# Performance work log

Hardware: AMD Instinct MI355X
Metric: run time of the kernel (lower is better)

The kernel has to match this reference:

```python
import jax, jax.numpy as jnp
import numpy as np

EPS = 1e-5


def _whiten(X, T):
    # X: (B, C, H, W); group whitening with g=1, d=C, m=B*H*W
    B, C, H, W = X.shape
    g, d = 1, C
    x = jnp.transpose(X, (1, 0, 2, 3)).reshape(g, d, -1)  # (g, d, m)
    m = x.shape[-1]
    mean = jnp.mean(x, axis=-1, keepdims=True)
    xc = x - mean
    I = jnp.broadcast_to(jnp.eye(d, dtype=X.dtype)[None], (g, d, d))
    Sigma = EPS * I + jnp.einsum('gim,gjm->gij', xc, xc) / m
    rTr = 1.0 / jnp.trace(Sigma, axis1=1, axis2=2)[:, None, None]  # 1/tr(Sigma)
    Sigma_N = Sigma * rTr
    P = I
    for _ in range(T):  # Newton-Schulz: P <- 1.5*P - 0.5*P^3 @ Sigma_N
        P = 1.5 * P - 0.5 * (P @ P @ P @ Sigma_N)
    wm = P * jnp.sqrt(rTr)  # inverse sqrt of Sigma
    xn = jnp.einsum('gij,gjm->gim', wm, xc)  # (g, d, m)
    return jnp.transpose(xn.reshape(C, B, H, W), (1, 0, 2, 3))


def reference(X, rot, T):
    # mode = -1: whiten then rotate with running_rot, affine=False
    B, C, H, W = X.shape
    g = rot.shape[0]
    d = C // g
    Xn = _whiten(X, T)                       # (B, C, H, W)
    Xh = Xn.reshape(B, g, d, H, W)
    Xr = jnp.einsum('bgchw,gdc->bgdhw', Xh, rot)
    return Xr.reshape(B, C, H, W)


def setup_inputs() -> dict:
    key = jax.random.key(0)
    k1, k2 = jax.random.split(key)
    X = jax.random.normal(k1, (32, 512, 56, 56), dtype=jnp.float32)
    # running_rot buffer; use a random orthogonal matrix for realism
    A = jax.random.normal(k2, (512, 512), dtype=jnp.float32)
    Q, _ = jnp.linalg.qr(A)
    rot = Q[None]  # (1, 512, 512)
    return {"X": X, "rot": rot, "T": 10}
```

## Files before the change

### kernel.cpp

```cpp
#include <hip/hip_runtime.h>
#include <hip/hip_bf16.h>

typedef __bf16 v8bf __attribute__((ext_vector_type(8)));
typedef float  v4f  __attribute__((ext_vector_type(4)));
typedef unsigned short u16;
typedef unsigned int   u32;

#define GAS __attribute__((address_space(1)))
#define LAS __attribute__((address_space(3)))

constexpr int C_ = 512;
constexpr int S_ = 3136;
constexpr int B_ = 32;
constexpr int M_ = B_ * S_;
constexpr float INV_M = 1.0f / (float)M_;

__device__ __forceinline__ void async16(const u16* g, u16* l) {
  __builtin_amdgcn_global_load_lds((const GAS u32*)g, (LAS u32*)l, 16, 0, 0);
}

__device__ __forceinline__ u16 f2bf(float f) {
  u32 u = __builtin_bit_cast(u32, f);
  u += 0x7fffu + ((u >> 16) & 1u);
  return (u16)(u >> 16);
}
__device__ __forceinline__ float bf2f(u16 h) {
  u32 u = ((u32)h) << 16;
  return __builtin_bit_cast(float, u);
}

__global__ __launch_bounds__(256) void prep_kernel(const float* __restrict__ X,
        u16* __restrict__ xbf, u16* __restrict__ xbfT, float* __restrict__ chsum) {
  __shared__ u16 Ts[64 * 65];
  const int tid = threadIdx.x;
  const int s0 = blockIdx.x * 64;
  const int c0 = blockIdx.y * 64;
  const int b  = blockIdx.z;

  const int i  = tid >> 2;
  const int jc = (tid & 3) * 16;
  const float* xp = X + (b * C_ + c0 + i) * S_ + s0 + jc;
  u16* op = xbf + (c0 + i) * M_ + b * S_ + s0 + jc;
  float ssum = 0.f;
  #pragma unroll
  for (int u = 0; u < 4; ++u) {
    float4 xv = *(const float4*)(xp + u * 4);
    ssum += xv.x + xv.y + xv.z + xv.w;
    u16 e0 = f2bf(xv.x), e1 = f2bf(xv.y), e2 = f2bf(xv.z), e3 = f2bf(xv.w);
    *(ushort4*)(op + u * 4) = make_ushort4(e0, e1, e2, e3);
    const int lb = i * 65 + jc + u * 4;
    Ts[lb + 0] = e0; Ts[lb + 1] = e1; Ts[lb + 2] = e2; Ts[lb + 3] = e3;
  }
  ssum += __shfl_down(ssum, 2, 4);
  ssum += __shfl_down(ssum, 1, 4);
  if ((tid & 3) == 0) atomicAdd(&chsum[c0 + i], ssum);
  __syncthreads();

  const int lane = tid & 63, wv = tid >> 6;
  #pragma unroll
  for (int p = 0; p < 2; ++p) {
    const int j  = p * 32 + wv * 8 + (lane >> 3);
    const int cc = (lane & 7) * 8;
    u16 tmp[8];
    #pragma unroll
    for (int e = 0; e < 8; ++e) tmp[e] = Ts[(cc + e) * 65 + j];
    u16* tp = xbfT + (b * S_ + s0 + j) * C_ + c0 + cc;
    *(ushort4*)(tp + 0) = make_ushort4(tmp[0], tmp[1], tmp[2], tmp[3]);
    *(ushort4*)(tp + 4) = make_ushort4(tmp[4], tmp[5], tmp[6], tmp[7]);
  }
}

__global__ __launch_bounds__(256, 2) void sigma_gemm(const u16* __restrict__ xbf,
                                                     float* __restrict__ part) {
  __shared__ u16 As[128 * 64];
  __shared__ u16 Bs[128 * 64];
  const int tid = threadIdx.x;
  const int bid = blockIdx.x;
  const int z = bid & 31;
  const int t = bid >> 5;
  const int ti = (t >= 9) ? 3 : (t >= 7) ? 2 : (t >= 4) ? 1 : 0;
  const int tb = (t >= 9) ? 9 : (t >= 7) ? 7 : (t >= 4) ? 4 : 0;
  const int tj = ti + (t - tb);
  const int kbase = z * S_;
  const int srow = tid >> 3;
  const int scol = (tid & 7) * 8;
  const int lane = tid & 63, wv = tid >> 6;
  const int wm = (wv & 1) * 64, wn = (wv >> 1) * 64;
  const int lr = lane & 15, lq = lane >> 4;
  const u16* gA = xbf + (ti * 128) * M_ + kbase + scol;
  const u16* gB = xbf + (tj * 128) * M_ + kbase + scol;
  v4f acc[4][4] = {};
  for (int it = 0; it < 49; ++it) {
    const int k0 = it * 64;
    #pragma unroll
    for (int q = 0; q < 4; ++q) {
      const int r = q * 32 + srow;
      async16(gA + r * M_ + k0, &As[r * 64 + scol]);
      async16(gB + r * M_ + k0, &Bs[r * 64 + scol]);
    }
    __syncthreads();
    #pragma unroll
    for (int kk = 0; kk < 2; ++kk) {
      v8bf a[4], b[4];
      #pragma unroll
      for (int x = 0; x < 4; ++x) a[x] = *(const v8bf*)&As[(wm + x*16 + lr)*64 + kk*32 + lq*8];
      #pragma unroll
      for (int x = 0; x < 4; ++x) b[x] = *(const v8bf*)&Bs[(wn + x*16 + lr)*64 + kk*32 + lq*8];
      #pragma unroll
      for (int mi = 0; mi < 4; ++mi)
        #pragma unroll
        for (int ni = 0; ni < 4; ++ni)
          acc[mi][ni] = __builtin_amdgcn_mfma_f32_16x16x32_bf16(a[mi], b[ni], acc[mi][ni], 0, 0, 0);
    }
    __syncthreads();
  }
  float* op = part + (size_t)(z * 10 + t) * (128 * 128);
  #pragma unroll
  for (int mi = 0; mi < 4; ++mi) {
    const int li = wm + mi * 16 + lq * 4;
    #pragma unroll
    for (int ni = 0; ni < 4; ++ni) {
      const int lj = wn + ni * 16 + lr;
      #pragma unroll
      for (int r = 0; r < 4; ++r)
        op[(li + r) * 128 + lj] = acc[mi][ni][r];
    }
  }
}

__global__ __launch_bounds__(256) void reduce_sigma(const float* __restrict__ part,
        const float* __restrict__ chsum, float* __restrict__ Sigma,
        float* __restrict__ trace) {
  const int idx = blockIdx.x * 256 + threadIdx.x;
  const int t = idx >> 14;
  const int r = idx & 16383;
  const int ii = r >> 7, jj = r & 127;
  const int ti = (t >= 9) ? 3 : (t >= 7) ? 2 : (t >= 4) ? 1 : 0;
  const int tb = (t >= 9) ? 9 : (t >= 7) ? 7 : (t >= 4) ? 4 : 0;
  const int tj = ti + (t - tb);
  const int i = ti * 128 + ii, j = tj * 128 + jj;
  float s = 0.f;
  #pragma unroll 8
  for (int z = 0; z < 32; ++z) s += part[(size_t)(z * 10 + t) * 16384 + r];
  float val = s * INV_M - (chsum[i] * INV_M) * (chsum[j] * INV_M);
  if (i == j) val += 1e-5f;
  Sigma[i * 512 + j] = val;
  if (i != j) Sigma[j * 512 + i] = val;
  if (i == j) atomicAdd(trace, val);
}

__global__ __launch_bounds__(256) void init_ns(const float* __restrict__ Sigma,
        const float* __restrict__ trace, const float* __restrict__ rot,
        u16* __restrict__ SNhi, u16* __restrict__ SNlo,
        float* __restrict__ P, u16* __restrict__ Phi, u16* __restrict__ Plo,
        u16* __restrict__ rothi, u16* __restrict__ rotlo) {
  const int idx = blockIdx.x * 256 + threadIdx.x;
  const float rtr = 1.0f / trace[0];
  const float sn = Sigma[idx] * rtr;
  u16 h = f2bf(sn);
  SNhi[idx] = h; SNlo[idx] = f2bf(sn - bf2f(h));
  const bool diag = (idx >> 9) == (idx & 511);
  P[idx] = diag ? 1.0f : 0.f;
  Phi[idx] = diag ? (u16)0x3F80 : (u16)0;
  Plo[idx] = 0;
  const float rv = rot[idx];
  u16 rh = f2bf(rv);
  rothi[idx] = rh; rotlo[idx] = f2bf(rv - bf2f(rh));
}

__global__ __launch_bounds__(256) void ns_mm(
    const u16* __restrict__ Ahi, const u16* __restrict__ Alo,
    const u16* __restrict__ B0hi, const u16* __restrict__ B0lo,
    const u16* __restrict__ B1hi, const u16* __restrict__ B1lo,
    u16* __restrict__ C0hi, u16* __restrict__ C0lo,
    u16* __restrict__ C1hi, u16* __restrict__ C1lo,
    float* __restrict__ P, const float* __restrict__ trace,
    float* __restrict__ M2f, u16* __restrict__ M2bf,
    const int* __restrict__ Tptr, int iter, int mode) {
  if (Tptr && iter >= Tptr[0]) return;
  __shared__ u16 Ah[64 * 64];
  __shared__ u16 Al[64 * 64];
  __shared__ u16 Bh[64 * 64];
  __shared__ u16 Bl[64 * 64];
  const int tid = threadIdx.x;
  const int tj = blockIdx.x, ti = blockIdx.y, zb = blockIdx.z;
  const u16* Bhip = zb ? B1hi : B0hi;
  const u16* Blop = zb ? B1lo : B0lo;
  const int r  = tid >> 3;
  const int sg = tid & 7;
  const int swz = (sg ^ (r & 7)) * 8;
  const int lofs = r * 64 + sg * 8;
  const u16* gAh = Ahi  + (ti * 64 + r) * 512 + swz;
  const u16* gAl = Alo  + (ti * 64 + r) * 512 + swz;
  const u16* gBh = Bhip + (tj * 64 + r) * 512 + swz;
  const u16* gBl = Blop + (tj * 64 + r) * 512 + swz;
  const int lane = tid & 63, wv = tid >> 6;
  const int wr = wv >> 1, wc = wv & 1;
  const int lr = lane & 15, lq = lane >> 4;
  v4f acc[2][2] = {};
  for (int it = 0; it < 8; ++it) {
    const int k0 = it * 64;
    async16(gAh + k0,            &Ah[lofs]);
    async16(gAh + k0 + 32 * 512, &Ah[lofs + 32 * 64]);
    async16(gAl + k0,            &Al[lofs]);
    async16(gAl + k0 + 32 * 512, &Al[lofs + 32 * 64]);
    async16(gBh + k0,            &Bh[lofs]);
    async16(gBh + k0 + 32 * 512, &Bh[lofs + 32 * 64]);
    async16(gBl + k0,            &Bl[lofs]);
    async16(gBl + k0 + 32 * 512, &Bl[lofs + 32 * 64]);
    __syncthreads();
    #pragma unroll
    for (int kk = 0; kk < 2; ++kk) {
      v8bf ah[2], al[2], bh[2], bl[2];
      const int col = ((kk * 4 + lq) ^ (lr & 7)) * 8;
      #pragma unroll
      for (int x = 0; x < 2; ++x) {
        const int rowA = (wr * 32 + x * 16 + lr) * 64;
        ah[x] = *(const v8bf*)&Ah[rowA + col];
        al[x] = *(const v8bf*)&Al[rowA + col];
        const int rowB = (wc * 32 + x * 16 + lr) * 64;
        bh[x] = *(const v8bf*)&Bh[rowB + col];
        bl[x] = *(const v8bf*)&Bl[rowB + col];
      }
      #pragma unroll
      for (int mi = 0; mi < 2; ++mi)
        #pragma unroll
        for (int ni = 0; ni < 2; ++ni) {
          acc[mi][ni] = __builtin_amdgcn_mfma_f32_16x16x32_bf16(ah[mi], bh[ni], acc[mi][ni], 0, 0, 0);
          acc[mi][ni] = __builtin_amdgcn_mfma_f32_16x16x32_bf16(ah[mi], bl[ni], acc[mi][ni], 0, 0, 0);
          acc[mi][ni] = __builtin_amdgcn_mfma_f32_16x16x32_bf16(al[mi], bh[ni], acc[mi][ni], 0, 0, 0);
        }
    }
    __syncthreads();
  }
  u16* Chi = zb ? C1hi : C0hi;
  u16* Clo = zb ? C1lo : C0lo;
  const float sc = (mode == 2) ? sqrtf(1.0f / trace[0]) : 0.f;
  #pragma unroll
  for (int mi = 0; mi < 2; ++mi) {
    const int gr0 = ti * 64 + wr * 32 + mi * 16 + lq * 4;
    #pragma unroll
    for (int ni = 0; ni < 2; ++ni) {
      const int gc = tj * 64 + wc * 32 + ni * 16 + lr;
      #pragma unroll
      for (int q = 0; q < 4; ++q) {
        const int o = (gr0 + q) * 512 + gc;
        const float vv = acc[mi][ni][q];
        if (mode == 0) {
          u16 h = f2bf(vv);
          Chi[o] = h; Clo[o] = f2bf(vv - bf2f(h));
        } else if (mode == 1) {
          const float nv = 1.5f * P[o] - 0.5f * vv;
          P[o] = nv;
          u16 h = f2bf(nv);
          Chi[o] = h; Clo[o] = f2bf(nv - bf2f(h));
        } else {
          const float w = vv * sc;
          M2f[o] = w; M2bf[o] = f2bf(w);
        }
      }
    }
  }
}

__global__ __launch_bounds__(256) void calc_v(const float* __restrict__ M2f,
        const float* __restrict__ chsum, float* __restrict__ v) {
  const int d = blockIdx.x * 256 + threadIdx.x;
  float s = 0.f;
  for (int c = 0; c < 512; ++c) s += M2f[d * 512 + c] * (chsum[c] * INV_M);
  v[d] = s;
}

__global__ __launch_bounds__(256, 2) void out_gemm(const u16* __restrict__ Abf,
        const u16* __restrict__ Bt, const float* __restrict__ v, float* __restrict__ out) {
  __shared__ u16 As[128 * 64];
  __shared__ u16 Bs[128 * 64];
  const int tid = threadIdx.x;
  const int tn = blockIdx.x, td = blockIdx.y;
  const int srow = tid >> 3, scol = (tid & 7) * 8;
  const int lane = tid & 63, wv = tid >> 6;
  const int wm = (wv & 1) * 64, wn = (wv >> 1) * 64;
  const int lr = lane & 15, lq = lane >> 4;
  const u16* gA = Abf + (td * 128) * 512 + scol;
  const u16* gB = Bt + (tn * 128) * 512 + scol;
  v4f acc[4][4] = {};
  for (int it = 0; it < 8; ++it) {
    const int k0 = it * 64;
    #pragma unroll
    for (int q = 0; q < 4; ++q) {
      const int r = q * 32 + srow;
      async16(gA + r * 512 + k0, &As[r * 64 + scol]);
      async16(gB + r * 512 + k0, &Bs[r * 64 + scol]);
    }
    __syncthreads();
    #pragma unroll
    for (int kk = 0; kk < 2; ++kk) {
      v8bf a[4], b[4];
      #pragma unroll
      for (int x = 0; x < 4; ++x) a[x] = *(const v8bf*)&As[(wm + x*16 + lr)*64 + kk*32 + lq*8];
      #pragma unroll
      for (int x = 0; x < 4; ++x) b[x] = *(const v8bf*)&Bs[(wn + x*16 + lr)*64 + kk*32 + lq*8];
      #pragma unroll
      for (int mi = 0; mi < 4; ++mi)
        #pragma unroll
        for (int ni = 0; ni < 4; ++ni)
          acc[mi][ni] = __builtin_amdgcn_mfma_f32_16x16x32_bf16(a[mi], b[ni], acc[mi][ni], 0, 0, 0);
    }
    __syncthreads();
  }
  #pragma unroll
  for (int mi = 0; mi < 4; ++mi) {
    const int d0 = td * 128 + wm + mi * 16 + lq * 4;
    const float vd0 = v[d0 + 0], vd1 = v[d0 + 1], vd2 = v[d0 + 2], vd3 = v[d0 + 3];
    #pragma unroll
    for (int ni = 0; ni < 4; ++ni) {
      const unsigned mcol = tn * 128 + wn + ni * 16 + lr;
      const unsigned bb = mcol / 3136u;
      const unsigned ss = mcol - bb * 3136u;
      const int obase = (int)(bb * 512u) * 3136 + (int)ss;
      out[obase + (d0 + 0) * 3136] = acc[mi][ni][0] - vd0;
      out[obase + (d0 + 1) * 3136] = acc[mi][ni][1] - vd1;
      out[obase + (d0 + 2) * 3136] = acc[mi][ni][2] - vd2;
      out[obase + (d0 + 3) * 3136] = acc[mi][ni][3] - vd3;
    }
  }
}

extern "C" void kernel_launch(void* const* d_in, const int* in_sizes, int n_in,
                              void* d_out, int out_size, void* d_ws, size_t ws_size,
                              hipStream_t stream) {
  const float* X   = (const float*)d_in[0];
  const float* rot = (const float*)d_in[1];
  const int*   T   = (const int*)d_in[2];
  float* out = (float*)d_out;

  char* ws = (char*)d_ws;
  size_t off = 0;
  auto alloc = [&](size_t bytes) -> char* {
    char* p = ws + off;
    off += (bytes + 255) & ~(size_t)255;
    return p;
  };
  u16*   xbf   = (u16*)alloc((size_t)C_ * M_ * 2);
  u16*   xbfT  = (u16*)alloc((size_t)M_ * C_ * 2);
  float* part  = (float*)alloc((size_t)320 * 16384 * 4);
  float* Sigma = (float*)alloc((size_t)C_ * C_ * 4);
  float* P     = (float*)alloc((size_t)C_ * C_ * 4);
  float* M2f   = (float*)alloc((size_t)C_ * C_ * 4);
  u16*   SNhi  = (u16*)alloc((size_t)C_ * C_ * 2);
  u16*   SNlo  = (u16*)alloc((size_t)C_ * C_ * 2);
  u16*   Phi   = (u16*)alloc((size_t)C_ * C_ * 2);
  u16*   Plo   = (u16*)alloc((size_t)C_ * C_ * 2);
  u16*   T1hi  = (u16*)alloc((size_t)C_ * C_ * 2);
  u16*   T1lo  = (u16*)alloc((size_t)C_ * C_ * 2);
  u16*   T2hi  = (u16*)alloc((size_t)C_ * C_ * 2);
  u16*   T2lo  = (u16*)alloc((size_t)C_ * C_ * 2);
  u16*   rothi = (u16*)alloc((size_t)C_ * C_ * 2);
  u16*   rotlo = (u16*)alloc((size_t)C_ * C_ * 2);
  u16*   M2bf  = (u16*)alloc((size_t)C_ * C_ * 2);
  float* chsum = (float*)alloc(2048);
  float* trace = (float*)alloc(256);
  float* v     = (float*)alloc(2048);
  (void)ws_size; (void)in_sizes; (void)n_in; (void)out_size;

  hipMemsetAsync(chsum, 0, 2048 + 256, stream);

  prep_kernel<<<dim3(49, 8, 32), 256, 0, stream>>>(X, xbf, xbfT, chsum);
  sigma_gemm<<<dim3(320), 256, 0, stream>>>(xbf, part);
  reduce_sigma<<<dim3(640), 256, 0, stream>>>(part, chsum, Sigma, trace);
  init_ns<<<dim3(1024), 256, 0, stream>>>(Sigma, trace, rot, SNhi, SNlo, P, Phi, Plo, rothi, rotlo);

  for (int iter = 0; iter < 10; ++iter) {
    ns_mm<<<dim3(8, 8, 2), 256, 0, stream>>>(Phi, Plo, Phi, Plo, SNhi, SNlo,
        T1hi, T1lo, T2hi, T2lo, P, trace, M2f, M2bf, T, iter, 0);
    ns_mm<<<dim3(8, 8, 1), 256, 0, stream>>>(T1hi, T1lo, T2hi, T2lo, nullptr, nullptr,
        Phi, Plo, nullptr, nullptr, P, trace, M2f, M2bf, T, iter, 1);
  }
  ns_mm<<<dim3(8, 8, 1), 256, 0, stream>>>(rothi, rotlo, Phi, Plo, nullptr, nullptr,
      Phi, Plo, nullptr, nullptr, P, trace, M2f, M2bf, nullptr, 0, 2);
  calc_v<<<dim3(2), 256, 0, stream>>>(M2f, chsum, v);
  out_gemm<<<dim3(784, 4), 256, 0, stream>>>(M2bf, xbfT, v, out);
}
```

Before: 805.0 us.

## Fuse Newton-Schulz iterations into one cooperative kernel with grid syncs

Replaces the reduce_sigma, init_ns, the twenty ns_mm launches and calc_v with a single cooperative kernel of 128 blocks that uses grid.sync between phases. The first Newton-Schulz iteration is folded analytically into initialization (P1 = 1.5I - 0.5*Sigma_N), which skips two matmuls. calc_v becomes a wave-parallel reduction with shuffles. The aim is to remove per-launch overhead and tail gaps in the small 512x512 iteration chain, at the cost of grid-wide barriers and half the blocks idling during single-output matmul phases.

```diff
diff --git a/kernel.cpp b/kernel.cpp
--- a/kernel.cpp
+++ b/kernel.cpp
@@ -1,5 +1,8 @@
 #include <hip/hip_runtime.h>
 #include <hip/hip_bf16.h>
+#include <hip/hip_cooperative_groups.h>
+
+namespace cg = cooperative_groups;
 
 typedef __bf16 v8bf __attribute__((ext_vector_type(8)));
 typedef float  v4f  __attribute__((ext_vector_type(4)));
@@ -128,78 +131,32 @@
   }
 }
 
-__global__ __launch_bounds__(256) void reduce_sigma(const float* __restrict__ part,
-        const float* __restrict__ chsum, float* __restrict__ Sigma,
-        float* __restrict__ trace) {
-  const int idx = blockIdx.x * 256 + threadIdx.x;
-  const int t = idx >> 14;
-  const int r = idx & 16383;
-  const int ii = r >> 7, jj = r & 127;
-  const int ti = (t >= 9) ? 3 : (t >= 7) ? 2 : (t >= 4) ? 1 : 0;
-  const int tb = (t >= 9) ? 9 : (t >= 7) ? 7 : (t >= 4) ? 4 : 0;
-  const int tj = ti + (t - tb);
-  const int i = ti * 128 + ii, j = tj * 128 + jj;
-  float s = 0.f;
-  #pragma unroll 8
-  for (int z = 0; z < 32; ++z) s += part[(size_t)(z * 10 + t) * 16384 + r];
-  float val = s * INV_M - (chsum[i] * INV_M) * (chsum[j] * INV_M);
-  if (i == j) val += 1e-5f;
-  Sigma[i * 512 + j] = val;
-  if (i != j) Sigma[j * 512 + i] = val;
-  if (i == j) atomicAdd(trace, val);
-}
-
-__global__ __launch_bounds__(256) void init_ns(const float* __restrict__ Sigma,
-        const float* __restrict__ trace, const float* __restrict__ rot,
-        u16* __restrict__ SNhi, u16* __restrict__ SNlo,
-        float* __restrict__ P, u16* __restrict__ Phi, u16* __restrict__ Plo,
-        u16* __restrict__ rothi, u16* __restrict__ rotlo) {
-  const int idx = blockIdx.x * 256 + threadIdx.x;
-  const float rtr = 1.0f / trace[0];
-  const float sn = Sigma[idx] * rtr;
-  u16 h = f2bf(sn);
-  SNhi[idx] = h; SNlo[idx] = f2bf(sn - bf2f(h));
-  const bool diag = (idx >> 9) == (idx & 511);
-  P[idx] = diag ? 1.0f : 0.f;
-  Phi[idx] = diag ? (u16)0x3F80 : (u16)0;
-  Plo[idx] = 0;
-  const float rv = rot[idx];
-  u16 rh = f2bf(rv);
-  rothi[idx] = rh; rotlo[idx] = f2bf(rv - bf2f(rh));
-}
-
-__global__ __launch_bounds__(256) void ns_mm(
+__device__ void mm64(
     const u16* __restrict__ Ahi, const u16* __restrict__ Alo,
-    const u16* __restrict__ B0hi, const u16* __restrict__ B0lo,
-    const u16* __restrict__ B1hi, const u16* __restrict__ B1lo,
-    u16* __restrict__ C0hi, u16* __restrict__ C0lo,
-    u16* __restrict__ C1hi, u16* __restrict__ C1lo,
-    float* __restrict__ P, const float* __restrict__ trace,
-    float* __restrict__ M2f, u16* __restrict__ M2bf,
-    const int* __restrict__ Tptr, int iter, int mode) {
-  if (Tptr && iter >= Tptr[0]) return;
+    const u16* __restrict__ Bhi, const u16* __restrict__ Blo,
+    int ti, int tj, int mode,
+    u16* __restrict__ Chi, u16* __restrict__ Clo,
+    float* __restrict__ P, float sc,
+    float* __restrict__ M2f, u16* __restrict__ M2bf) {
   __shared__ u16 Ah[64 * 64];
   __shared__ u16 Al[64 * 64];
   __shared__ u16 Bh[64 * 64];
   __shared__ u16 Bl[64 * 64];
   const int tid = threadIdx.x;
-  const int tj = blockIdx.x, ti = blockIdx.y, zb = blockIdx.z;
-  const u16* Bhip = zb ? B1hi : B0hi;
-  const u16* Blop = zb ? B1lo : B0lo;
   const int r  = tid >> 3;
   const int sg = tid & 7;
   const int swz = (sg ^ (r & 7)) * 8;
   const int lofs = r * 64 + sg * 8;
-  const u16* gAh = Ahi  + (ti * 64 + r) * 512 + swz;
-  const u16* gAl = Alo  + (ti * 64 + r) * 512 + swz;
-  const u16* gBh = Bhip + (tj * 64 + r) * 512 + swz;
-  const u16* gBl = Blop + (tj * 64 + r) * 512 + swz;
+  const u16* gAh = Ahi + (ti * 64 + r) * 512 + swz;
+  const u16* gAl = Alo + (ti * 64 + r) * 512 + swz;
+  const u16* gBh = Bhi + (tj * 64 + r) * 512 + swz;
+  const u16* gBl = Blo + (tj * 64 + r) * 512 + swz;
   const int lane = tid & 63, wv = tid >> 6;
   const int wr = wv >> 1, wc = wv & 1;
   const int lr = lane & 15, lq = lane >> 4;
   v4f acc[2][2] = {};
-  for (int it = 0; it < 8; ++it) {
-    const int k0 = it * 64;
+  for (int itk = 0; itk < 8; ++itk) {
+    const int k0 = itk * 64;
     async16(gAh + k0,            &Ah[lofs]);
     async16(gAh + k0 + 32 * 512, &Ah[lofs + 32 * 64]);
     async16(gAl + k0,            &Al[lofs]);
@@ -233,9 +190,6 @@
     }
     __syncthreads();
   }
-  u16* Chi = zb ? C1hi : C0hi;
-  u16* Clo = zb ? C1lo : C0lo;
-  const float sc = (mode == 2) ? sqrtf(1.0f / trace[0]) : 0.f;
   #pragma unroll
   for (int mi = 0; mi < 2; ++mi) {
     const int gr0 = ti * 64 + wr * 32 + mi * 16 + lq * 4;
@@ -263,12 +217,92 @@
   }
 }
 
-__global__ __launch_bounds__(256) void calc_v(const float* __restrict__ M2f,
-        const float* __restrict__ chsum, float* __restrict__ v) {
-  const int d = blockIdx.x * 256 + threadIdx.x;
-  float s = 0.f;
-  for (int c = 0; c < 512; ++c) s += M2f[d * 512 + c] * (chsum[c] * INV_M);
-  v[d] = s;
+__global__ __launch_bounds__(256) void ns_coop(
+    const float* __restrict__ part, const float* __restrict__ chsum,
+    float* __restrict__ Sigma, float* __restrict__ trace,
+    const float* __restrict__ rot,
+    u16* __restrict__ SNhi, u16* __restrict__ SNlo,
+    u16* __restrict__ Phi,  u16* __restrict__ Plo,
+    u16* __restrict__ T1hi, u16* __restrict__ T1lo,
+    u16* __restrict__ T2hi, u16* __restrict__ T2lo,
+    u16* __restrict__ rothi, u16* __restrict__ rotlo,
+    float* __restrict__ P, float* __restrict__ M2f, u16* __restrict__ M2bf,
+    float* __restrict__ v, const int* __restrict__ Tptr) {
+  cg::grid_group grid = cg::this_grid();
+  const int bid = blockIdx.x;
+  const int tid = threadIdx.x;
+  const int gidx0 = bid * 256 + tid;
+
+  for (int idx = gidx0; idx < 10 * 16384; idx += 128 * 256) {
+    const int t = idx >> 14;
+    const int rr = idx & 16383;
+    const int ii = rr >> 7, jj = rr & 127;
+    const int ti = (t >= 9) ? 3 : (t >= 7) ? 2 : (t >= 4) ? 1 : 0;
+    const int tb = (t >= 9) ? 9 : (t >= 7) ? 7 : (t >= 4) ? 4 : 0;
+    const int tj = ti + (t - tb);
+    const int i = ti * 128 + ii, j = tj * 128 + jj;
+    float s = 0.f;
+    #pragma unroll 8
+    for (int z = 0; z < 32; ++z) s += part[(size_t)(z * 10 + t) * 16384 + rr];
+    float val = s * INV_M - (chsum[i] * INV_M) * (chsum[j] * INV_M);
+    if (i == j) val += 1e-5f;
+    Sigma[i * 512 + j] = val;
+    if (i != j) Sigma[j * 512 + i] = val;
+    if (i == j) atomicAdd(trace, val);
+  }
+  grid.sync();
+
+  const float rtr = 1.0f / trace[0];
+  const int Tval = Tptr[0];
+
+  for (int idx = gidx0; idx < 512 * 512; idx += 128 * 256) {
+    const float sn = Sigma[idx] * rtr;
+    u16 h = f2bf(sn);
+    SNhi[idx] = h; SNlo[idx] = f2bf(sn - bf2f(h));
+    const bool diag = (idx >> 9) == (idx & 511);
+    const float p0 = (Tval > 0) ? ((diag ? 1.5f : 0.f) - 0.5f * sn)
+                                : (diag ? 1.0f : 0.f);
+    P[idx] = p0;
+    u16 ph = f2bf(p0);
+    Phi[idx] = ph; Plo[idx] = f2bf(p0 - bf2f(ph));
+    const float rv = rot[idx];
+    u16 rh = f2bf(rv);
+    rothi[idx] = rh; rotlo[idx] = f2bf(rv - bf2f(rh));
+  }
+  grid.sync();
+
+  for (int it = 1; it < Tval; ++it) {
+    {
+      const int job = bid & 63, zb = bid >> 6;
+      mm64(Phi, Plo, zb ? SNhi : Phi, zb ? SNlo : Plo,
+           job >> 3, job & 7, 0,
+           zb ? T2hi : T1hi, zb ? T2lo : T1lo, P, 0.f, M2f, M2bf);
+    }
+    grid.sync();
+    if (bid < 64) {
+      mm64(T1hi, T1lo, T2hi, T2lo, bid >> 3, bid & 7, 1,
+           Phi, Plo, P, 0.f, M2f, M2bf);
+    }
+    grid.sync();
+  }
+
+  if (bid < 64) {
+    mm64(rothi, rotlo, Phi, Plo, bid >> 3, bid & 7, 2,
+         nullptr, nullptr, P, sqrtf(rtr), M2f, M2bf);
+  }
+  grid.sync();
+
+  {
+    const int d = bid * 4 + (tid >> 6);
+    const int lane = tid & 63;
+    float s = 0.f;
+    for (int c = lane; c < 512; c += 64)
+      s += M2f[d * 512 + c] * (chsum[c] * INV_M);
+    s += __shfl_down(s, 32); s += __shfl_down(s, 16);
+    s += __shfl_down(s, 8);  s += __shfl_down(s, 4);
+    s += __shfl_down(s, 2);  s += __shfl_down(s, 1);
+    if (lane == 0) v[d] = s;
+  }
 }
 
 __global__ __launch_bounds__(256, 2) void out_gemm(const u16* __restrict__ Abf,
@@ -367,17 +401,16 @@
 
   prep_kernel<<<dim3(49, 8, 32), 256, 0, stream>>>(X, xbf, xbfT, chsum);
   sigma_gemm<<<dim3(320), 256, 0, stream>>>(xbf, part);
-  reduce_sigma<<<dim3(640), 256, 0, stream>>>(part, chsum, Sigma, trace);
-  init_ns<<<dim3(1024), 256, 0, stream>>>(Sigma, trace, rot, SNhi, SNlo, P, Phi, Plo, rothi, rotlo);
-
-  for (int iter = 0; iter < 10; ++iter) {
-    ns_mm<<<dim3(8, 8, 2), 256, 0, stream>>>(Phi, Plo, Phi, Plo, SNhi, SNlo,
-        T1hi, T1lo, T2hi, T2lo, P, trace, M2f, M2bf, T, iter, 0);
-    ns_mm<<<dim3(8, 8, 1), 256, 0, stream>>>(T1hi, T1lo, T2hi, T2lo, nullptr, nullptr,
-        Phi, Plo, nullptr, nullptr, P, trace, M2f, M2bf, T, iter, 1);
-  }
-  ns_mm<<<dim3(8, 8, 1), 256, 0, stream>>>(rothi, rotlo, Phi, Plo, nullptr, nullptr,
-      Phi, Plo, nullptr, nullptr, P, trace, M2f, M2bf, nullptr, 0, 2);
-  calc_v<<<dim3(2), 256, 0, stream>>>(M2f, chsum, v);
+
+  void* args[] = {
+    (void*)&part, (void*)&chsum, (void*)&Sigma, (void*)&trace,
+    (void*)&rot,
+    (void*)&SNhi, (void*)&SNlo, (void*)&Phi, (void*)&Plo,
+    (void*)&T1hi, (void*)&T1lo, (void*)&T2hi, (void*)&T2lo,
+    (void*)&rothi, (void*)&rotlo,
+    (void*)&P, (void*)&M2f, (void*)&M2bf, (void*)&v, (void*)&T
+  };
+  hipLaunchCooperativeKernel(ns_coop, dim3(128), dim3(256), args, 0, stream);
+
   out_gemm<<<dim3(784, 4), 256, 0, stream>>>(M2bf, xbfT, v, out);
 }
```

Result: slower. 1.041 ms (+29.3%).
